# Performance work log

Measured on AMD Instinct MI355X. Metric: run time of the kernel, lower is better.

## Reference

```python
import jax, jax.numpy as jnp
import numpy as np

FS = 16000
M = 800            # win_length = 0.05*fs
K = 1024           # n_fft = next pow2
HOP = 600          # M - V, V = M//4
NBINS = 256        # 4000*K//fs
L_MAX = 13         # round(0.5*fs/hop)
L_MIN = 3
MIN_DB = 10.0
DEFAULT_RT60 = 0.5
EPS = 1e-10
INVALID = 1e30


def _stft_power(y):
    # y: [B,1,T] -> power spectrogram [B,1,NBINS,nF] (torchaudio Spectrogram, power=2,
    # center=True reflect pad, periodic hann of length M zero-padded centered to K)
    n = jnp.arange(M, dtype=y.dtype)
    win = 0.5 - 0.5 * jnp.cos(2.0 * jnp.pi * n / M)
    w = jnp.zeros(K, dtype=y.dtype).at[(K - M) // 2:(K - M) // 2 + M].set(win)
    yp = jnp.pad(y, ((0, 0), (0, 0), (K // 2, K // 2)), mode='reflect')
    nF = 1 + (yp.shape[-1] - K) // HOP
    idx = jnp.arange(nF)[:, None] * HOP + jnp.arange(K)[None, :]
    frames = yp[..., idx] * w                       # [B,1,nF,K]
    spec = jnp.abs(jnp.fft.rfft(frames)) ** 2       # [B,1,nF,K//2+1]
    return jnp.swapaxes(spec, -1, -2)[..., :NBINS, :]


def reference(y, coeffs):
    Y = _stft_power(y)                              # [B,1,F,T]
    B = Y.shape[0]
    T = Y.shape[-1]
    Yf = Y.reshape(B, -1, T)                        # [B,F,T] (mono channel folded)

    # --- strictly-decreasing run detection for every window length L in [3,13] ---
    d = (jnp.diff(Yf, axis=-1) < 0).astype(jnp.int32)                      # [B,F,T-1]
    c = jnp.concatenate([jnp.zeros_like(d[..., :1]), jnp.cumsum(d, -1)], -1)  # [B,F,T]
    Ls = jnp.arange(L_MIN, L_MAX + 1)               # [11]
    t = jnp.arange(T)
    end = jnp.minimum(t[None, :] + Ls[:, None] - 1, T - 1)                 # [11,T]
    cnt = jnp.take(c, end, axis=-1) - c[:, :, None, :]                     # [B,F,11,T]
    valid_t = (t[None, :] + Ls[:, None]) <= T                              # [11,T]
    dec = (cnt == (Ls - 1)[None, None, :, None]) & valid_t[None, None]     # [B,F,11,T]

    # per subband: largest L with any decreasing window (compute_individual_masks)
    hasL = dec.any(-1)                              # [B,F,11]
    chosen = (Ls.shape[0] - 1) - jnp.argmax(hasL[..., ::-1], -1)           # [B,F]
    has_any = hasL.any(-1)                          # [B,F]
    start_mask = jnp.take_along_axis(dec, chosen[..., None, None], axis=2)[:, :, 0, :]
    start_mask = start_mask & has_any[..., None]    # [B,F,T]
    lenL = L_MIN + chosen                           # [B,F] window length per subband

    # --- padded windows of length L_MAX for every start position ---
    widx = jnp.clip(t[:, None] + jnp.arange(L_MAX)[None, :], 0, T - 1)     # [T,13]
    W = jnp.take(Yf, widx, axis=-1)                 # [B,F,T,13]
    lm = (jnp.arange(L_MAX) < lenL[..., None])[:, :, None, :]              # [B,F,1,13]
    lmf = lm.astype(W.dtype)

    # EDC = reversed cumsum of power, in dB, rescaled to start at 0
    wm = W * lmf
    edc = jnp.cumsum(wm[..., ::-1], -1)[..., ::-1]
    edc_db = 10.0 * jnp.log10(jnp.maximum(edc, EPS))
    scaled = edc_db - edc_db[..., :1]               # [B,F,T,13]

    last_idx = jnp.broadcast_to((lenL - 1)[:, :, None, None], scaled.shape[:-1] + (1,))
    last = jnp.take_along_axis(scaled, last_idx, -1)[..., 0]               # [B,F,T]
    selected = last < -MIN_DB

    x = jnp.arange(L_MAX, dtype=scaled.dtype)
    nl = lenL.astype(scaled.dtype)[..., None]       # [B,F,1]
    xm = jnp.sum(x * lmf[:, :, 0, :], -1, keepdims=True) / nl              # [B,F,1]
    ym = jnp.sum(scaled * lmf, -1) / nl             # [B,F,T]
    xc = (x - xm[..., None]) * lmf                  # [B,F,1,13]
    num = jnp.sum(xc * (scaled - ym[..., None]), -1)                        # [B,F,T]
    den = jnp.sum(xc * xc, -1)                      # [B,F,1]
    slope = num / den

    valid = start_mask & selected
    slope_safe = jnp.where(valid, slope, -1.0)
    rt60 = (-60.0 / slope_safe) * (HOP / FS)        # [B,F,T]

    # per-batch lower median over all valid segments (torch.median semantics)
    vals = jnp.where(valid, rt60, INVALID).reshape(B, -1)
    nvalid = valid.reshape(B, -1).sum(-1)
    srt = jnp.sort(vals, -1)
    midx = jnp.maximum((nvalid - 1) // 2, 0)
    med = jnp.take_along_axis(srt, midx[:, None], -1)[:, 0]
    med = jnp.where(nvalid > 0, med, 0.0)

    corr = coeffs[0] + coeffs[1] * med              # degree-1 polynomial correction
    out = jnp.where(nvalid > 0, corr, DEFAULT_RT60)
    out = jnp.maximum(out, 0.01)
    return out[:, None, None]                       # [B,1,1]


def setup_inputs() -> dict:
    key = jax.random.key(0)
    k1, _ = jax.random.split(key)
    y = jax.random.normal(k1, (32, 1, 160000), dtype=jnp.float32)
    coeffs = jnp.array([0.0, 1.0], dtype=jnp.float32)  # identity polynomial init
    return {"y": y, "coeffs": coeffs}
```

## Files before the change

### kernel.cpp

```cpp
#include <hip/hip_runtime.h>
#include <hip/hip_bf16.h>
#include <math.h>

#define NB 32
#define TLEN 160000
#define KFFT 1024
#define HOP 600
#define NBINS 256
#define TT 267
#define NROWS (NB * NBINS)
#define LMAX 13
#define LMIN 3

__device__ __forceinline__ unsigned f2key(float f) {
    unsigned b = __float_as_uint(f);
    return (b & 0x80000000u) ? ~b : (b | 0x80000000u);
}

__device__ __forceinline__ int P(int i) { return i + (i >> 4); }

__global__ void init_kernel(float2* __restrict__ tw, float* __restrict__ wtab) {
    int j = blockIdx.x * blockDim.x + threadIdx.x;
    if (j < 512) {
        double ang = -2.0 * 3.14159265358979323846 * (double)j / 1024.0;
        tw[j] = make_float2((float)cos(ang), (float)sin(ang));
    }
    if (j < 800) {
        float arg = (6.2831855f * (float)j) / 800.0f;
        wtab[j] = 0.5f - 0.5f * cosf(arg);
    }
}

__global__ __launch_bounds__(256) void stft_power_kernel(
        const float* __restrict__ y, const float2* __restrict__ twg,
        const float* __restrict__ wtab, float* __restrict__ Y) {
    __shared__ float2 z[2][1024 + 64];
    __shared__ float2 twl[512 + 32];

    const int g = blockIdx.x;
    const int b = blockIdx.y;
    const int tid = threadIdx.x;
    const int f0 = 4 * g;

    for (int j = tid; j < 512; j += 256) twl[P(j)] = twg[j];

    const float* yb = y + (size_t)b * TLEN;
    #pragma unroll
    for (int a = 0; a < 2; ++a) {
        const int fa = f0 + 2 * a;
        const bool hasB = (fa + 1 < TT);
        const int base = fa * HOP - 512;
        for (int i = tid; i < 1024; i += 256) {
            float v0 = 0.0f, v1 = 0.0f;
            if (i >= 112 && i < 912) {
                float w = wtab[i - 112];
                int p0 = base + i;
                int q0 = p0 < 0 ? -p0 : (p0 >= TLEN ? 2 * TLEN - 2 - p0 : p0);
                v0 = yb[q0] * w;
                if (hasB) {
                    int p1 = p0 + HOP;
                    int q1 = p1 < 0 ? -p1 : (p1 >= TLEN ? 2 * TLEN - 2 - p1 : p1);
                    v1 = yb[q1] * w;
                }
            }
            z[a][P(i)] = make_float2(v0, v1);
        }
    }
    __syncthreads();

    #pragma unroll
    for (int s = 8; s >= 0; s -= 2) {
        const int q = 1 << s;
        const int j = tid & (q - 1);
        const int i0 = ((tid >> s) << (s + 2)) | j;
        const float2 u  = twl[P(j << (8 - s))];
        const float2 w2 = twl[P(j << (9 - s))];
        #pragma unroll
        for (int a = 0; a < 2; ++a) {
            float2 a0 = z[a][P(i0)];
            float2 a1 = z[a][P(i0 + q)];
            float2 a2 = z[a][P(i0 + 2 * q)];
            float2 a3 = z[a][P(i0 + 3 * q)];
            float b0r = a0.x + a2.x, b0i = a0.y + a2.y;
            float b1r = a1.x + a3.x, b1i = a1.y + a3.y;
            float t2r = a0.x - a2.x, t2i = a0.y - a2.y;
            float t3r = a1.x - a3.x, t3i = a1.y - a3.y;
            float b2r = t2r * u.x - t2i * u.y, b2i = t2r * u.y + t2i * u.x;
            float m3r = t3r * u.x - t3i * u.y, m3i = t3r * u.y + t3i * u.x;
            float b3r = m3i, b3i = -m3r;
            float2 c0 = make_float2(b0r + b1r, b0i + b1i);
            float d1r = b0r - b1r, d1i = b0i - b1i;
            float2 c1 = make_float2(d1r * w2.x - d1i * w2.y, d1r * w2.y + d1i * w2.x);
            float2 c2 = make_float2(b2r + b3r, b2i + b3i);
            float d3r = b2r - b3r, d3i = b2i - b3i;
            float2 c3 = make_float2(d3r * w2.x - d3i * w2.y, d3r * w2.y + d3i * w2.x);
            z[a][P(i0)]         = c0;
            z[a][P(i0 + q)]     = c1;
            z[a][P(i0 + 2 * q)] = c2;
            z[a][P(i0 + 3 * q)] = c3;
        }
        __syncthreads();
    }

    const int k = tid;
    const int nk = (1024 - k) & 1023;
    const int rk = (int)(__brev((unsigned)k) >> 22);
    const int rn = (int)(__brev((unsigned)nk) >> 22);
    #pragma unroll
    for (int a = 0; a < 2; ++a) {
        const int fa = f0 + 2 * a;
        float2 zk = z[a][P(rk)], zn = z[a][P(rn)];
        float x0r = 0.5f * (zk.x + zn.x), x0i = 0.5f * (zk.y - zn.y);
        float x1r = 0.5f * (zk.y + zn.y), x1i = 0.5f * (zn.x - zk.x);
        float* yrow = Y + ((size_t)b * NBINS + k) * TT;
        yrow[fa] = x0r * x0r + x0i * x0i;
        if (fa + 1 < TT) yrow[fa + 1] = x1r * x1r + x1i * x1i;
    }
}

__global__ __launch_bounds__(256) void subband_kernel(
        const float* __restrict__ Y, unsigned* __restrict__ compact,
        int* __restrict__ rowcnt) {
    __shared__ float ys[4][272];

    const int tid = threadIdx.x;
    const int lane = tid & 63;
    const int wave = tid >> 6;
    const int row = blockIdx.x * 4 + wave;
    const float* src = Y + (size_t)row * TT;

    float v[5];
    #pragma unroll
    for (int c = 0; c < 5; ++c) {
        int t = c * 64 + lane;
        v[c] = (t < TT) ? src[t] : 0.0f;
        if (t < TT) ys[wave][t] = v[c];
    }
    __syncthreads();

    const float* yy = ys[wave];

    unsigned long long m[5];
    #pragma unroll
    for (int c = 0; c < 5; ++c) {
        int t = c * 64 + lane;
        bool d = (t < TT - 1) && (yy[t + 1] < v[c]);
        m[c] = __ballot(d);
    }

    auto runl = [&](int c, int l) -> int {
        unsigned long long lo = m[c] >> l;
        if (l && c < 4) lo |= m[c + 1] << (64 - l);
        unsigned win = (unsigned)lo & 0xFFFu;
        return (win == 0xFFFu) ? 12 : (__ffs((int)~win) - 1);
    };

    int rl[5];
    int mx = 0;
    #pragma unroll
    for (int c = 0; c < 5; ++c) { rl[c] = runl(c, lane); mx = max(mx, rl[c]); }
    #pragma unroll
    for (int o = 32; o; o >>= 1) mx = max(mx, __shfl_xor(mx, o));
    const int maxrun = mx;

    if (maxrun < 2) {
        if (lane == 0) rowcnt[row] = 0;
        return;
    }
    const int L = maxrun + 1;

    float sumx = 0.0f;
    #pragma unroll
    for (int j = 0; j < LMAX; ++j) if (j < L) sumx += (float)j;
    const float xm = sumx / (float)L;
    float den = 0.0f;
    #pragma unroll
    for (int j = 0; j < LMAX; ++j) if (j < L) { float xc = (float)j - xm; den += xc * xc; }

    unsigned keys[5];
    unsigned long long vm[5];
    #pragma unroll
    for (int c = 0; c < 5; ++c) {
        const int t = c * 64 + lane;
        bool sel = false;
        unsigned key = 0u;
        if (rl[c] >= L - 1) {
            float edc[LMAX];
            float s = 0.0f;
            #pragma unroll
            for (int j = LMAX - 1; j >= 0; --j) {
                if (j < L) s += yy[t + j];
                edc[j] = s;
            }
            float db0 = 10.0f * log10f(fmaxf(edc[0], 1e-10f));
            float scl[LMAX];
            float s1 = 0.0f;
            float last = 0.0f;
            #pragma unroll
            for (int j = 0; j < LMAX; ++j) {
                if (j < L) {
                    float db = 10.0f * log10f(fmaxf(edc[j], 1e-10f));
                    float sc = db - db0;
                    scl[j] = sc;
                    s1 += sc;
                    if (j == L - 1) last = sc;
                }
            }
            if (last < -10.0f) {
                const float ym = s1 / (float)L;
                float num = 0.0f;
                #pragma unroll
                for (int j = 0; j < LMAX; ++j)
                    if (j < L) num += ((float)j - xm) * (scl[j] - ym);
                const float slope = num / den;
                float rt60 = (-60.0f / slope) * 0.0375f;
                sel = true;
                key = f2key(rt60);
            }
        }
        vm[c] = __ballot(sel);
        keys[c] = key;
    }

    unsigned* dst = compact + (size_t)row * TT;
    const unsigned long long below = (1ull << lane) - 1ull;
    int base = 0;
    #pragma unroll
    for (int c = 0; c < 5; ++c) {
        if (vm[c] & (1ull << lane))
            dst[base + (int)__popcll(vm[c] & below)] = keys[c];
        base += (int)__popcll(vm[c]);
    }
    if (lane == 0) rowcnt[row] = base;
}

__global__ __launch_bounds__(256) void median_kernel(
        const unsigned* __restrict__ compact, const int* __restrict__ rowcnt,
        const float* __restrict__ coeffs, float* __restrict__ out) {
    __shared__ unsigned hist[16384];
    __shared__ unsigned wsum[4];
    __shared__ int sh_sel;
    __shared__ unsigned sh_kkc;
    __shared__ unsigned sh_kk, sh_prefix, sh_pmask;
    __shared__ int sh_n;

    const int b = blockIdx.x;
    const int tid = threadIdx.x;
    const int lane = tid & 63;
    const int wave = tid >> 6;
    const int myrow = b * NBINS + tid;
    const int myc = rowcnt[myrow];
    const unsigned* mykeys = compact + (size_t)myrow * TT;

    {
        unsigned x = (unsigned)myc;
        #pragma unroll
        for (int o = 1; o < 64; o <<= 1) { unsigned t = __shfl_up(x, o); if (lane >= o) x += t; }
        if (lane == 63) wsum[wave] = x;
        __syncthreads();
        if (tid == 0) {
            int n = (int)(wsum[0] + wsum[1] + wsum[2] + wsum[3]);
            sh_n = n;
            sh_kk = (n > 0) ? (unsigned)((n - 1) / 2) : 0u;
            sh_prefix = 0u; sh_pmask = 0u;
        }
        __syncthreads();
    }
    const int n = sh_n;
    if (n == 0) {
        if (tid == 0) out[b] = 0.5f;
        return;
    }

    const int shifts[3] = {18, 4, 0};
    for (int p = 0; p < 3; ++p) {
        const int shift = shifts[p];
        const bool big = (p < 2);

        if (big) {
            uint4* h4 = (uint4*)hist;
            for (int i = tid; i < 4096; i += 256) h4[i] = make_uint4(0u, 0u, 0u, 0u);
        } else if (tid < 16) hist[tid] = 0u;
        __syncthreads();

        const unsigned pfx = sh_prefix, pm = sh_pmask;
        const unsigned bmask = big ? 16383u : 15u;
        for (int i = 0; i < myc; ++i) {
            unsigned k = mykeys[i];
            if ((k & pm) == pfx) atomicAdd(&hist[(k >> shift) & bmask], 1u);
        }
        __syncthreads();

        const unsigned kk = sh_kk;
        if (big) {
            unsigned s = 0;
            const int base = tid * 64;
            #pragma unroll 8
            for (int ii = 0; ii < 64; ++ii) s += hist[base + ((ii + tid) & 63)];
            unsigned x = s;
            #pragma unroll
            for (int o = 1; o < 64; o <<= 1) { unsigned t = __shfl_up(x, o); if (lane >= o) x += t; }
            if (lane == 63) wsum[wave] = x;
            __syncthreads();
            unsigned woff = 0;
            for (int w = 0; w < wave; ++w) woff += wsum[w];
            const unsigned incl = x + woff, excl = incl - s;
            if (kk >= excl && kk < incl) { sh_sel = tid; sh_kkc = kk - excl; }
            __syncthreads();
            const int sel = sh_sel;
            const unsigned kkc = sh_kkc;
            if (wave == 0) {
                unsigned h = hist[sel * 64 + lane];
                unsigned xx = h;
                #pragma unroll
                for (int o = 1; o < 64; o <<= 1) { unsigned t = __shfl_up(xx, o); if (lane >= o) xx += t; }
                unsigned ex = xx - h;
                if (kkc >= ex && kkc < xx) {
                    sh_prefix = pfx | ((unsigned)(sel * 64 + lane) << shift);
                    sh_pmask  = pm | (16383u << shift);
                    sh_kk = kkc - ex;
                }
            }
            __syncthreads();
        } else {
            if (wave == 0) {
                unsigned h = (lane < 16) ? hist[lane] : 0u;
                unsigned xx = h;
                #pragma unroll
                for (int o = 1; o < 64; o <<= 1) { unsigned t = __shfl_up(xx, o); if (lane >= o) xx += t; }
                unsigned ex = xx - h;
                if (lane < 16 && kk >= ex && kk < xx)
                    sh_prefix = pfx | (unsigned)lane;
            }
            __syncthreads();
        }
    }

    if (tid == 0) {
        unsigned kx = sh_prefix;
        unsigned fb = (kx & 0x80000000u) ? (kx & 0x7FFFFFFFu) : ~kx;
        float med = __uint_as_float(fb);
        out[b] = fmaxf(coeffs[0] + coeffs[1] * med, 0.01f);
    }
}

extern "C" void kernel_launch(void* const* d_in, const int* in_sizes, int n_in,
                              void* d_out, int out_size, void* d_ws, size_t ws_size,
                              hipStream_t stream) {
    const float* y = (const float*)d_in[0];
    const float* coeffs = (const float*)d_in[1];
    float* out = (float*)d_out;

    const size_t YB = (size_t)NROWS * TT * sizeof(float);
    char* base = (char*)d_ws;
    float* Y = (float*)base;
    unsigned* compact = (unsigned*)(base + YB);
    int* rowcnt = (int*)(base + 2 * YB);
    float2* tw = (float2*)(base + 2 * YB + (size_t)NROWS * sizeof(int));
    float* wtab = (float*)((char*)tw + 512 * sizeof(float2));

    init_kernel<<<4, 256, 0, stream>>>(tw, wtab);
    stft_power_kernel<<<dim3((TT + 3) / 4, NB), 256, 0, stream>>>(y, tw, wtab, Y);
    subband_kernel<<<NROWS / 4, 256, 0, stream>>>(Y, compact, rowcnt);
    median_kernel<<<NB, 256, 0, stream>>>(compact, rowcnt, coeffs, out);
}
```

Baseline: 115.3 us.

## Restructure STFT FFT into register-resident radix-16 passes with more frames per block

The STFT kernel now processes 8 frames per block (4 packed complex FFTs), one per wavefront. The FFT is restructured from five shared-memory radix-4 stages, each followed by a block barrier, into two register-resident 16-point passes plus a final radix-4 pass. Shared memory uses an XOR swizzle, frame loads use vectorized float4 reads on the interior fast path, and the Y rows are padded to an even length so results can be stored as float2 pairs. This cuts LDS traffic and barriers, at the cost of higher register pressure and a larger shared footprint per block.

```diff
diff --git a/kernel.cpp b/kernel.cpp
--- a/kernel.cpp
+++ b/kernel.cpp
@@ -4,20 +4,24 @@
 
 #define NB 32
 #define TLEN 160000
-#define KFFT 1024
 #define HOP 600
 #define NBINS 256
 #define TT 267
+#define TTP 268
 #define NROWS (NB * NBINS)
 #define LMAX 13
-#define LMIN 3
 
 __device__ __forceinline__ unsigned f2key(float f) {
     unsigned b = __float_as_uint(f);
     return (b & 0x80000000u) ? ~b : (b | 0x80000000u);
 }
-
 __device__ __forceinline__ int P(int i) { return i + (i >> 4); }
+__device__ __forceinline__ int Q(int i) { return i ^ ((i >> 4) & 0x3C); }
+__device__ __forceinline__ float2 cmul(float2 a, float2 w) {
+    return make_float2(a.x * w.x - a.y * w.y, a.x * w.y + a.y * w.x);
+}
+__device__ __forceinline__ float2 cadd(float2 a, float2 b) { return make_float2(a.x + b.x, a.y + b.y); }
+__device__ __forceinline__ float2 csub(float2 a, float2 b) { return make_float2(a.x - b.x, a.y - b.y); }
 
 __global__ void init_kernel(float2* __restrict__ tw, float* __restrict__ wtab) {
     int j = blockIdx.x * blockDim.x + threadIdx.x;
@@ -34,87 +38,172 @@
 __global__ __launch_bounds__(256) void stft_power_kernel(
         const float* __restrict__ y, const float2* __restrict__ twg,
         const float* __restrict__ wtab, float* __restrict__ Y) {
-    __shared__ float2 z[2][1024 + 64];
-    __shared__ float2 twl[512 + 32];
+    __shared__ float2 zz[4][1024];
+    __shared__ float2 twl[544];
 
     const int g = blockIdx.x;
     const int b = blockIdx.y;
     const int tid = threadIdx.x;
-    const int f0 = 4 * g;
+    const int f0 = 8 * g;
 
     for (int j = tid; j < 512; j += 256) twl[P(j)] = twg[j];
 
     const float* yb = y + (size_t)b * TLEN;
     #pragma unroll
-    for (int a = 0; a < 2; ++a) {
+    for (int a = 0; a < 4; ++a) {
         const int fa = f0 + 2 * a;
+        if (fa >= TT) break;
         const bool hasB = (fa + 1 < TT);
         const int base = fa * HOP - 512;
-        for (int i = tid; i < 1024; i += 256) {
-            float v0 = 0.0f, v1 = 0.0f;
+        const int i = 4 * tid;
+        float2 q4[4];
+        if (base >= 0 && hasB) {
             if (i >= 112 && i < 912) {
-                float w = wtab[i - 112];
-                int p0 = base + i;
-                int q0 = p0 < 0 ? -p0 : (p0 >= TLEN ? 2 * TLEN - 2 - p0 : p0);
-                v0 = yb[q0] * w;
-                if (hasB) {
-                    int p1 = p0 + HOP;
-                    int q1 = p1 < 0 ? -p1 : (p1 >= TLEN ? 2 * TLEN - 2 - p1 : p1);
-                    v1 = yb[q1] * w;
+                float4 w4 = *(const float4*)(wtab + (i - 112));
+                float4 a0 = *(const float4*)(yb + base + i);
+                float4 a1 = *(const float4*)(yb + base + HOP + i);
+                q4[0] = make_float2(a0.x * w4.x, a1.x * w4.x);
+                q4[1] = make_float2(a0.y * w4.y, a1.y * w4.y);
+                q4[2] = make_float2(a0.z * w4.z, a1.z * w4.z);
+                q4[3] = make_float2(a0.w * w4.w, a1.w * w4.w);
+            } else {
+                q4[0] = q4[1] = q4[2] = q4[3] = make_float2(0.f, 0.f);
+            }
+        } else {
+            #pragma unroll
+            for (int m = 0; m < 4; ++m) {
+                const int ii = i + m;
+                float v0 = 0.f, v1 = 0.f;
+                if (ii >= 112 && ii < 912) {
+                    float w = wtab[ii - 112];
+                    int p0 = base + ii;
+                    int q0 = p0 < 0 ? -p0 : p0;
+                    v0 = yb[q0] * w;
+                    if (hasB) v1 = yb[p0 + HOP] * w;
                 }
-            }
-            z[a][P(i)] = make_float2(v0, v1);
-        }
+                q4[m] = make_float2(v0, v1);
+            }
+        }
+        float4* dst = (float4*)&zz[a][Q(i)];
+        dst[0] = make_float4(q4[0].x, q4[0].y, q4[1].x, q4[1].y);
+        dst[1] = make_float4(q4[2].x, q4[2].y, q4[3].x, q4[3].y);
     }
     __syncthreads();
 
-    #pragma unroll
-    for (int s = 8; s >= 0; s -= 2) {
-        const int q = 1 << s;
-        const int j = tid & (q - 1);
-        const int i0 = ((tid >> s) << (s + 2)) | j;
-        const float2 u  = twl[P(j << (8 - s))];
-        const float2 w2 = twl[P(j << (9 - s))];
-        #pragma unroll
-        for (int a = 0; a < 2; ++a) {
-            float2 a0 = z[a][P(i0)];
-            float2 a1 = z[a][P(i0 + q)];
-            float2 a2 = z[a][P(i0 + 2 * q)];
-            float2 a3 = z[a][P(i0 + 3 * q)];
-            float b0r = a0.x + a2.x, b0i = a0.y + a2.y;
-            float b1r = a1.x + a3.x, b1i = a1.y + a3.y;
-            float t2r = a0.x - a2.x, t2i = a0.y - a2.y;
-            float t3r = a1.x - a3.x, t3i = a1.y - a3.y;
-            float b2r = t2r * u.x - t2i * u.y, b2i = t2r * u.y + t2i * u.x;
-            float m3r = t3r * u.x - t3i * u.y, m3i = t3r * u.y + t3i * u.x;
-            float b3r = m3i, b3i = -m3r;
-            float2 c0 = make_float2(b0r + b1r, b0i + b1i);
-            float d1r = b0r - b1r, d1i = b0i - b1i;
-            float2 c1 = make_float2(d1r * w2.x - d1i * w2.y, d1r * w2.y + d1i * w2.x);
-            float2 c2 = make_float2(b2r + b3r, b2i + b3i);
-            float d3r = b2r - b3r, d3i = b2i - b3i;
-            float2 c3 = make_float2(d3r * w2.x - d3i * w2.y, d3r * w2.y + d3i * w2.x);
-            z[a][P(i0)]         = c0;
-            z[a][P(i0 + q)]     = c1;
-            z[a][P(i0 + 2 * q)] = c2;
-            z[a][P(i0 + 3 * q)] = c3;
-        }
-        __syncthreads();
-    }
+    {
+        const int a = tid >> 6, j = tid & 63;
+        float2 x[16];
+        #pragma unroll
+        for (int k = 0; k < 16; ++k) x[k] = zz[a][Q(j + 64 * k)];
+        #pragma unroll
+        for (int k = 0; k < 8; ++k) {
+            float2 s = csub(x[k], x[k + 8]);
+            x[k] = cadd(x[k], x[k + 8]);
+            x[k + 8] = cmul(s, twl[P(j + 64 * k)]);
+        }
+        #pragma unroll
+        for (int h = 0; h < 16; h += 8)
+            #pragma unroll
+            for (int k = 0; k < 4; ++k) {
+                float2 s = csub(x[h + k], x[h + k + 4]);
+                x[h + k] = cadd(x[h + k], x[h + k + 4]);
+                x[h + k + 4] = cmul(s, twl[P(2 * j + 128 * k)]);
+            }
+        #pragma unroll
+        for (int h = 0; h < 16; h += 4)
+            #pragma unroll
+            for (int k = 0; k < 2; ++k) {
+                float2 s = csub(x[h + k], x[h + k + 2]);
+                x[h + k] = cadd(x[h + k], x[h + k + 2]);
+                x[h + k + 2] = cmul(s, twl[P(4 * j + 256 * k)]);
+            }
+        {
+            const float2 wD = twl[P(8 * j)];
+            #pragma unroll
+            for (int h = 0; h < 16; h += 2) {
+                float2 s = csub(x[h], x[h + 1]);
+                x[h] = cadd(x[h], x[h + 1]);
+                x[h + 1] = cmul(s, wD);
+            }
+        }
+        #pragma unroll
+        for (int k = 0; k < 16; ++k) zz[a][Q(j + 64 * k)] = x[k];
+    }
+    __syncthreads();
+
+    {
+        const int a = tid >> 6, l = tid & 63;
+        const int gg = l >> 2, j2 = l & 3;
+        const int b0 = 64 * gg + j2;
+        float2 x[16];
+        #pragma unroll
+        for (int k = 0; k < 16; ++k) x[k] = zz[a][Q(b0 + 4 * k)];
+        #pragma unroll
+        for (int k = 0; k < 8; ++k) {
+            float2 s = csub(x[k], x[k + 8]);
+            x[k] = cadd(x[k], x[k + 8]);
+            x[k + 8] = cmul(s, twl[P(16 * j2 + 64 * k)]);
+        }
+        #pragma unroll
+        for (int h = 0; h < 16; h += 8)
+            #pragma unroll
+            for (int k = 0; k < 4; ++k) {
+                float2 s = csub(x[h + k], x[h + k + 4]);
+                x[h + k] = cadd(x[h + k], x[h + k + 4]);
+                x[h + k + 4] = cmul(s, twl[P(32 * j2 + 128 * k)]);
+            }
+        #pragma unroll
+        for (int h = 0; h < 16; h += 4)
+            #pragma unroll
+            for (int k = 0; k < 2; ++k) {
+                float2 s = csub(x[h + k], x[h + k + 2]);
+                x[h + k] = cadd(x[h + k], x[h + k + 2]);
+                x[h + k + 2] = cmul(s, twl[P(64 * (j2 + 4 * k))]);
+            }
+        {
+            const float2 wD = twl[P(128 * j2)];
+            #pragma unroll
+            for (int h = 0; h < 16; h += 2) {
+                float2 s = csub(x[h], x[h + 1]);
+                x[h] = cadd(x[h], x[h + 1]);
+                x[h + 1] = cmul(s, wD);
+            }
+        }
+        #pragma unroll
+        for (int k = 0; k < 16; ++k) zz[a][Q(b0 + 4 * k)] = x[k];
+    }
+    __syncthreads();
+
+    #pragma unroll
+    for (int a = 0; a < 4; ++a) {
+        float4* pp = (float4*)&zz[a][Q(4 * tid)];
+        float4 r0 = pp[0], r1 = pp[1];
+        float2 x0 = make_float2(r0.x, r0.y), x1 = make_float2(r0.z, r0.w);
+        float2 x2 = make_float2(r1.x, r1.y), x3 = make_float2(r1.z, r1.w);
+        float2 e0 = cadd(x0, x2);
+        float2 e1 = cadd(x1, x3);
+        float2 d0 = csub(x0, x2);
+        float2 d1 = csub(x1, x3);
+        float2 d1m = make_float2(d1.y, -d1.x);
+        pp[0] = make_float4(e0.x + e1.x, e0.y + e1.y, e0.x - e1.x, e0.y - e1.y);
+        pp[1] = make_float4(d0.x + d1m.x, d0.y + d1m.y, d0.x - d1m.x, d0.y - d1m.y);
+    }
+    __syncthreads();
 
     const int k = tid;
     const int nk = (1024 - k) & 1023;
     const int rk = (int)(__brev((unsigned)k) >> 22);
     const int rn = (int)(__brev((unsigned)nk) >> 22);
-    #pragma unroll
-    for (int a = 0; a < 2; ++a) {
+    float* yrow = Y + ((size_t)b * NBINS + k) * TTP;
+    #pragma unroll
+    for (int a = 0; a < 4; ++a) {
         const int fa = f0 + 2 * a;
-        float2 zk = z[a][P(rk)], zn = z[a][P(rn)];
+        if (fa >= TT) break;
+        float2 zk = zz[a][Q(rk)], zn = zz[a][Q(rn)];
         float x0r = 0.5f * (zk.x + zn.x), x0i = 0.5f * (zk.y - zn.y);
         float x1r = 0.5f * (zk.y + zn.y), x1i = 0.5f * (zn.x - zk.x);
-        float* yrow = Y + ((size_t)b * NBINS + k) * TT;
-        yrow[fa] = x0r * x0r + x0i * x0i;
-        if (fa + 1 < TT) yrow[fa + 1] = x1r * x1r + x1i * x1i;
+        *(float2*)(yrow + fa) =
+            make_float2(x0r * x0r + x0i * x0i, x1r * x1r + x1i * x1i);
     }
 }
 
@@ -127,7 +216,7 @@
     const int lane = tid & 63;
     const int wave = tid >> 6;
     const int row = blockIdx.x * 4 + wave;
-    const float* src = Y + (size_t)row * TT;
+    const float* src = Y + (size_t)row * TTP;
 
     float v[5];
     #pragma unroll
@@ -222,7 +311,7 @@
         keys[c] = key;
     }
 
-    unsigned* dst = compact + (size_t)row * TT;
+    unsigned* dst = compact + (size_t)row * TTP;
     const unsigned long long below = (1ull << lane) - 1ull;
     int base = 0;
     #pragma unroll
@@ -250,7 +339,7 @@
     const int wave = tid >> 6;
     const int myrow = b * NBINS + tid;
     const int myc = rowcnt[myrow];
-    const unsigned* mykeys = compact + (size_t)myrow * TT;
+    const unsigned* mykeys = compact + (size_t)myrow * TTP;
 
     {
         unsigned x = (unsigned)myc;
@@ -351,7 +440,7 @@
     const float* coeffs = (const float*)d_in[1];
     float* out = (float*)d_out;
 
-    const size_t YB = (size_t)NROWS * TT * sizeof(float);
+    const size_t YB = (size_t)NROWS * TTP * sizeof(float);
     char* base = (char*)d_ws;
     float* Y = (float*)base;
     unsigned* compact = (unsigned*)(base + YB);
@@ -360,7 +449,7 @@
     float* wtab = (float*)((char*)tw + 512 * sizeof(float2));
 
     init_kernel<<<4, 256, 0, stream>>>(tw, wtab);
-    stft_power_kernel<<<dim3((TT + 3) / 4, NB), 256, 0, stream>>>(y, tw, wtab, Y);
+    stft_power_kernel<<<dim3((TT + 7) / 8, NB), 256, 0, stream>>>(y, tw, wtab, Y);
     subband_kernel<<<NROWS / 4, 256, 0, stream>>>(Y, compact, rowcnt);
     median_kernel<<<NB, 256, 0, stream>>>(compact, rowcnt, coeffs, out);
 }
```

Result: faster. 108.0 us (-6.3%).

## Do per-wave register FFT with shuffles and pad spectrogram rows

Applied to the files above, without the earlier changes.

The STFT kernel now gives each wavefront one pair of frames and runs the 1024-point FFT in registers. It uses 16 elements per lane and cross-lane shuffles for the last stages, which replaces the block-wide shared-memory radix-4 passes and their barriers. Spectrogram rows are padded to an even length so each frame pair is written as one float2 store. This removes the per-stage __syncthreads and shared-memory traffic, at the cost of higher register pressure. It also drops the upper reflect-padding branch, which relies on frames never running past the end of the signal.

```diff
diff --git a/kernel.cpp b/kernel.cpp
--- a/kernel.cpp
+++ b/kernel.cpp
@@ -4,20 +4,23 @@
 
 #define NB 32
 #define TLEN 160000
-#define KFFT 1024
 #define HOP 600
 #define NBINS 256
 #define TT 267
+#define TTP 268
 #define NROWS (NB * NBINS)
 #define LMAX 13
-#define LMIN 3
 
 __device__ __forceinline__ unsigned f2key(float f) {
     unsigned b = __float_as_uint(f);
     return (b & 0x80000000u) ? ~b : (b | 0x80000000u);
 }
-
 __device__ __forceinline__ int P(int i) { return i + (i >> 4); }
+__device__ __forceinline__ float2 cmul(float2 a, float2 w) {
+    return make_float2(a.x * w.x - a.y * w.y, a.x * w.y + a.y * w.x);
+}
+__device__ __forceinline__ float2 cadd(float2 a, float2 b) { return make_float2(a.x + b.x, a.y + b.y); }
+__device__ __forceinline__ float2 csub(float2 a, float2 b) { return make_float2(a.x - b.x, a.y - b.y); }
 
 __global__ void init_kernel(float2* __restrict__ tw, float* __restrict__ wtab) {
     int j = blockIdx.x * blockDim.x + threadIdx.x;
@@ -34,87 +37,124 @@
 __global__ __launch_bounds__(256) void stft_power_kernel(
         const float* __restrict__ y, const float2* __restrict__ twg,
         const float* __restrict__ wtab, float* __restrict__ Y) {
-    __shared__ float2 z[2][1024 + 64];
-    __shared__ float2 twl[512 + 32];
-
-    const int g = blockIdx.x;
+    __shared__ float2 twl[544];
+    __shared__ float2 zbin[4][1088];
+
+    const int tid = threadIdx.x;
+    const int lane = tid & 63;
+    const int wv = tid >> 6;
     const int b = blockIdx.y;
-    const int tid = threadIdx.x;
-    const int f0 = 4 * g;
 
     for (int j = tid; j < 512; j += 256) twl[P(j)] = twg[j];
+    __syncthreads();
+
+    const int wave_id = blockIdx.x * 4 + wv;
+    const int f0 = 2 * wave_id;
+    if (f0 >= TT) return;
+    const bool hasB = (f0 + 1 < TT);
 
     const float* yb = y + (size_t)b * TLEN;
-    #pragma unroll
-    for (int a = 0; a < 2; ++a) {
-        const int fa = f0 + 2 * a;
-        const bool hasB = (fa + 1 < TT);
-        const int base = fa * HOP - 512;
-        for (int i = tid; i < 1024; i += 256) {
-            float v0 = 0.0f, v1 = 0.0f;
-            if (i >= 112 && i < 912) {
-                float w = wtab[i - 112];
-                int p0 = base + i;
-                int q0 = p0 < 0 ? -p0 : (p0 >= TLEN ? 2 * TLEN - 2 - p0 : p0);
-                v0 = yb[q0] * w;
-                if (hasB) {
-                    int p1 = p0 + HOP;
-                    int q1 = p1 < 0 ? -p1 : (p1 >= TLEN ? 2 * TLEN - 2 - p1 : p1);
-                    v1 = yb[q1] * w;
-                }
-            }
-            z[a][P(i)] = make_float2(v0, v1);
-        }
-    }
-    __syncthreads();
-
-    #pragma unroll
-    for (int s = 8; s >= 0; s -= 2) {
-        const int q = 1 << s;
-        const int j = tid & (q - 1);
-        const int i0 = ((tid >> s) << (s + 2)) | j;
-        const float2 u  = twl[P(j << (8 - s))];
-        const float2 w2 = twl[P(j << (9 - s))];
-        #pragma unroll
-        for (int a = 0; a < 2; ++a) {
-            float2 a0 = z[a][P(i0)];
-            float2 a1 = z[a][P(i0 + q)];
-            float2 a2 = z[a][P(i0 + 2 * q)];
-            float2 a3 = z[a][P(i0 + 3 * q)];
-            float b0r = a0.x + a2.x, b0i = a0.y + a2.y;
-            float b1r = a1.x + a3.x, b1i = a1.y + a3.y;
-            float t2r = a0.x - a2.x, t2i = a0.y - a2.y;
-            float t3r = a1.x - a3.x, t3i = a1.y - a3.y;
-            float b2r = t2r * u.x - t2i * u.y, b2i = t2r * u.y + t2i * u.x;
-            float m3r = t3r * u.x - t3i * u.y, m3i = t3r * u.y + t3i * u.x;
-            float b3r = m3i, b3i = -m3r;
-            float2 c0 = make_float2(b0r + b1r, b0i + b1i);
-            float d1r = b0r - b1r, d1i = b0i - b1i;
-            float2 c1 = make_float2(d1r * w2.x - d1i * w2.y, d1r * w2.y + d1i * w2.x);
-            float2 c2 = make_float2(b2r + b3r, b2i + b3i);
-            float d3r = b2r - b3r, d3i = b2i - b3i;
-            float2 c3 = make_float2(d3r * w2.x - d3i * w2.y, d3r * w2.y + d3i * w2.x);
-            z[a][P(i0)]         = c0;
-            z[a][P(i0 + q)]     = c1;
-            z[a][P(i0 + 2 * q)] = c2;
-            z[a][P(i0 + 3 * q)] = c3;
-        }
-        __syncthreads();
-    }
-
-    const int k = tid;
-    const int nk = (1024 - k) & 1023;
-    const int rk = (int)(__brev((unsigned)k) >> 22);
-    const int rn = (int)(__brev((unsigned)nk) >> 22);
-    #pragma unroll
-    for (int a = 0; a < 2; ++a) {
-        const int fa = f0 + 2 * a;
-        float2 zk = z[a][P(rk)], zn = z[a][P(rn)];
+    const int base = f0 * HOP - 512;
+
+    float2 x[16];
+    #pragma unroll
+    for (int k = 0; k < 16; ++k) {
+        const int n = lane + 64 * k;
+        float v0 = 0.f, v1 = 0.f;
+        if (n >= 112 && n < 912) {
+            float w = wtab[n - 112];
+            int p0 = base + n;
+            int q0 = p0 < 0 ? -p0 : p0;
+            v0 = yb[q0] * w;
+            if (hasB) v1 = yb[p0 + HOP] * w;
+        }
+        x[k] = make_float2(v0, v1);
+    }
+
+    #pragma unroll
+    for (int k = 0; k < 8; ++k) {
+        float2 a = x[k], bb = x[k + 8];
+        x[k] = cadd(a, bb);
+        x[k + 8] = cmul(csub(a, bb), twl[P(lane + 64 * k)]);
+    }
+    #pragma unroll
+    for (int h = 0; h < 16; h += 8)
+        #pragma unroll
+        for (int k = 0; k < 4; ++k) {
+            float2 a = x[h + k], bb = x[h + k + 4];
+            x[h + k] = cadd(a, bb);
+            x[h + k + 4] = cmul(csub(a, bb), twl[P(2 * lane + 128 * k)]);
+        }
+    #pragma unroll
+    for (int h = 0; h < 16; h += 4)
+        #pragma unroll
+        for (int k = 0; k < 2; ++k) {
+            float2 a = x[h + k], bb = x[h + k + 2];
+            x[h + k] = cadd(a, bb);
+            x[h + k + 2] = cmul(csub(a, bb), twl[P(4 * lane + 256 * k)]);
+        }
+    {
+        const float2 wD = twl[P(8 * lane)];
+        #pragma unroll
+        for (int h = 0; h < 16; h += 2) {
+            float2 a = x[h], bb = x[h + 1];
+            x[h] = cadd(a, bb);
+            x[h + 1] = cmul(csub(a, bb), wD);
+        }
+    }
+
+    #pragma unroll
+    for (int st = 0; st < 4; ++st) {
+        const int dlt = 32 >> st;
+        const float2 wD = twl[P((16 << st) * (lane & (dlt - 1)))];
+        const bool upper = (lane & dlt) != 0;
+        #pragma unroll
+        for (int k = 0; k < 16; ++k) {
+            float2 p = make_float2(__shfl_xor(x[k].x, dlt), __shfl_xor(x[k].y, dlt));
+            x[k] = upper ? cmul(csub(p, x[k]), wD) : cadd(x[k], p);
+        }
+    }
+    {
+        const bool odd = (lane & 1) != 0;
+        const bool upper = (lane & 2) != 0;
+        #pragma unroll
+        for (int k = 0; k < 16; ++k) {
+            float2 p = make_float2(__shfl_xor(x[k].x, 2), __shfl_xor(x[k].y, 2));
+            if (!upper) x[k] = cadd(x[k], p);
+            else {
+                float2 d = csub(p, x[k]);
+                x[k] = odd ? make_float2(d.y, -d.x) : d;
+            }
+        }
+    }
+    {
+        const bool upper = (lane & 1) != 0;
+        #pragma unroll
+        for (int k = 0; k < 16; ++k) {
+            float2 p = make_float2(__shfl_xor(x[k].x, 1), __shfl_xor(x[k].y, 1));
+            x[k] = upper ? csub(p, x[k]) : cadd(x[k], p);
+        }
+    }
+
+    float2* zb = zbin[wv];
+    const int mrev = (int)(__brev((unsigned)lane) >> 26);
+    #pragma unroll
+    for (int k = 0; k < 16; ++k) {
+        const int slot = 16 * mrev + (int)(__brev((unsigned)k) >> 28);
+        zb[P(slot)] = x[k];
+    }
+
+    #pragma unroll
+    for (int c = 0; c < 4; ++c) {
+        const int bin = lane + 64 * c;
+        float2 zk = zb[P(bin)];
+        float2 zn = zb[P((1024 - bin) & 1023)];
         float x0r = 0.5f * (zk.x + zn.x), x0i = 0.5f * (zk.y - zn.y);
         float x1r = 0.5f * (zk.y + zn.y), x1i = 0.5f * (zn.x - zk.x);
-        float* yrow = Y + ((size_t)b * NBINS + k) * TT;
-        yrow[fa] = x0r * x0r + x0i * x0i;
-        if (fa + 1 < TT) yrow[fa + 1] = x1r * x1r + x1i * x1i;
+        float* pr = Y + ((size_t)b * NBINS + bin) * TTP + f0;
+        if (hasB) *(float2*)pr = make_float2(x0r * x0r + x0i * x0i,
+                                             x1r * x1r + x1i * x1i);
+        else      *pr = x0r * x0r + x0i * x0i;
     }
 }
 
@@ -127,7 +167,7 @@
     const int lane = tid & 63;
     const int wave = tid >> 6;
     const int row = blockIdx.x * 4 + wave;
-    const float* src = Y + (size_t)row * TT;
+    const float* src = Y + (size_t)row * TTP;
 
     float v[5];
     #pragma unroll
@@ -222,7 +262,7 @@
         keys[c] = key;
     }
 
-    unsigned* dst = compact + (size_t)row * TT;
+    unsigned* dst = compact + (size_t)row * TTP;
     const unsigned long long below = (1ull << lane) - 1ull;
     int base = 0;
     #pragma unroll
@@ -250,7 +290,7 @@
     const int wave = tid >> 6;
     const int myrow = b * NBINS + tid;
     const int myc = rowcnt[myrow];
-    const unsigned* mykeys = compact + (size_t)myrow * TT;
+    const unsigned* mykeys = compact + (size_t)myrow * TTP;
 
     {
         unsigned x = (unsigned)myc;
@@ -351,7 +391,7 @@
     const float* coeffs = (const float*)d_in[1];
     float* out = (float*)d_out;
 
-    const size_t YB = (size_t)NROWS * TT * sizeof(float);
+    const size_t YB = (size_t)NROWS * TTP * sizeof(float);
     char* base = (char*)d_ws;
     float* Y = (float*)base;
     unsigned* compact = (unsigned*)(base + YB);
@@ -360,7 +400,7 @@
     float* wtab = (float*)((char*)tw + 512 * sizeof(float2));
 
     init_kernel<<<4, 256, 0, stream>>>(tw, wtab);
-    stft_power_kernel<<<dim3((TT + 3) / 4, NB), 256, 0, stream>>>(y, tw, wtab, Y);
+    stft_power_kernel<<<dim3(34, NB), 256, 0, stream>>>(y, tw, wtab, Y);
     subband_kernel<<<NROWS / 4, 256, 0, stream>>>(Y, compact, rowcnt);
     median_kernel<<<NB, 256, 0, stream>>>(compact, rowcnt, coeffs, out);
 }
```

Result: slower. 118.7 us (+3.0%).
